# Performance work log

Hardware: AMD Instinct MI355X
Metric: run time of the kernel (lower is better)

## Reference

```python
import jax, jax.numpy as jnp
import numpy as np

B, T, E, H, V = 32, 120, 300, 256, 32000
C, G = 512, 7

def setup_inputs() -> dict:
    key = jax.random.key(0)
    ks = jax.random.split(key, 8)
    s = lambda k, shape, sc: (jax.random.normal(k, shape, jnp.float32) * sc)
    return {
        "features": jax.random.normal(ks[0], (B, C, G, G), jnp.float32),
        "embeddings": jax.random.normal(ks[1], (B, T, E), jnp.float32),
        "W_init": s(ks[2], (H, C), 0.04),          # nn.Linear(512, num_layers*H)
        "b_init": jnp.zeros((H,), jnp.float32),
        "W_fc2": s(ks[3], (H, C * G * G), 0.006),   # nn.Linear(512*49, H)
        "b_fc2": jnp.zeros((H,), jnp.float32),
        "W_ih": s(ks[4], (3 * H, E + H), 0.04),     # GRU weight_ih_l0 (r,z,n rows)
        "b_ih": jnp.zeros((3 * H,), jnp.float32),
        "W_hh": s(ks[5], (3 * H, H), 0.06),         # GRU weight_hh_l0
        "b_hh": jnp.zeros((3 * H,), jnp.float32),
        "W_fc": s(ks[6], (V, H), 0.06),             # nn.Linear(H, vocab)
        "b_fc": jnp.zeros((V,), jnp.float32),
        "length": T,
    }

def reference(features, embeddings, W_init, b_init, W_fc2, b_fc2,
              W_ih, b_ih, W_hh, b_hh, W_fc, b_fc, length):
    Bq, Cq = features.shape[0], features.shape[1]
    Hq = W_hh.shape[1]
    # init_hidden_state: [B,C,7,7] -> [B,49,C]
    f = jnp.transpose(features, (0, 2, 3, 1)).reshape(Bq, -1, Cq)
    h0 = f.mean(axis=1) @ W_init.T + b_init                      # [B,H], num_layers=1
    # flatten + fc2, broadcast over time, concat with embeddings
    feat = f.reshape(Bq, -1) @ W_fc2.T + b_fc2                   # [B,H]
    x = jnp.concatenate(
        [embeddings,
         jnp.broadcast_to(feat[:, None, :], (Bq, embeddings.shape[1], Hq))],
        axis=-1)                                                  # [B,T,E+H]
    xs = jnp.transpose(x[:, :length], (1, 0, 2))                  # [T,B,E+H]
    # precompute input-side gate projections for all timesteps (one big GEMM)
    gi = jnp.einsum('tbi,gi->tbg', xs, W_ih) + b_ih               # [T,B,3H]
    def step(h, g_x):
        g_h = h @ W_hh.T + b_hh
        r = jax.nn.sigmoid(g_x[..., :Hq] + g_h[..., :Hq])
        z = jax.nn.sigmoid(g_x[..., Hq:2 * Hq] + g_h[..., Hq:2 * Hq])
        n = jnp.tanh(g_x[..., 2 * Hq:] + r * g_h[..., 2 * Hq:])
        h_new = (1.0 - z) * n + z * h
        return h_new, h_new
    _, hs = jax.lax.scan(step, h0, gi)                            # [T,B,H]
    # per-step fc (dropout p=0.3 is identity in eval mode)
    logits = jnp.einsum('tbh,vh->btv', hs, W_fc) + b_fc           # [B,T,V]
    return logits
```

## Files before the change

### kernel.cpp

```cpp
#include <hip/hip_runtime.h>
#include <hip/hip_bf16.h>

#define BB 32
#define TT 120
#define EE 300
#define HH 256
#define VV 32000
#define CC 512
#define GG 49
#define KIN 556
#define CF 25088

typedef __attribute__((ext_vector_type(8))) short bf16x8;
typedef __attribute__((ext_vector_type(4))) float f32x4;

__device__ __forceinline__ float bpair_lo(unsigned int u) { return __uint_as_float(u << 16); }
__device__ __forceinline__ float bpair_hi(unsigned int u) { return __uint_as_float(u & 0xFFFF0000u); }

__device__ __forceinline__ unsigned int packbf(float a, float b) {
    union { __hip_bfloat16 h; unsigned short u; } ua, ub;
    ua.h = __float2bfloat16(a); ub.h = __float2bfloat16(b);
    return (unsigned int)ua.u | ((unsigned int)ub.u << 16);
}

#if defined(__has_builtin)
#  if __has_builtin(__builtin_amdgcn_fdot2_f32_bf16)
#    define USE_DOT2 1
#  endif
#endif
#ifndef USE_DOT2
#  define USE_DOT2 0
#endif

#if USE_DOT2
typedef __bf16 bf2_t __attribute__((ext_vector_type(2)));
__device__ __forceinline__ float dot2bf(unsigned int w, unsigned int h, float c) {
    return __builtin_amdgcn_fdot2_f32_bf16(__builtin_bit_cast(bf2_t, w),
                                           __builtin_bit_cast(bf2_t, h), c, false);
}
#else
__device__ __forceinline__ float dot2bf(unsigned int w, unsigned int h, float c) {
    c = fmaf(bpair_lo(w), bpair_lo(h), c);
    c = fmaf(bpair_hi(w), bpair_hi(h), c);
    return c;
}
#endif

__global__ void __launch_bounds__(256) k_pre(const float* __restrict__ features,
                                             const float* __restrict__ W_fc2,
                                             float* __restrict__ part,
                                             const float* __restrict__ W_hh,
                                             unsigned int* __restrict__ whh_bf,
                                             const float* __restrict__ W_init,
                                             const float* __restrict__ b_init,
                                             float* __restrict__ h0) {
    __shared__ float xs[98][BB];
    __shared__ float mf[CC];
    __shared__ float red[8][33];
    int bid = blockIdx.x;
    if (bid < 256) {
        int kc = bid;
        for (int idx = threadIdx.x; idx < 98 * BB; idx += 256) {
            int ii = idx >> 5, b = idx & 31;
            int ig = kc * 98 + ii;
            int c = ig & 511, p = ig >> 9;
            xs[ii][b] = features[(size_t)b * CF + c * GG + p];
        }
        __syncthreads();
        int h = threadIdx.x;
        float acc[BB];
#pragma unroll
        for (int b = 0; b < BB; ++b) acc[b] = 0.f;
        const float* wp = W_fc2 + (size_t)h * CF + kc * 98;
        for (int ii = 0; ii < 98; ii += 2) {
            float2 w2 = *(const float2*)(wp + ii);
            const float4* x0 = (const float4*)&xs[ii][0];
            const float4* x1 = (const float4*)&xs[ii + 1][0];
#pragma unroll
            for (int q = 0; q < 8; ++q) {
                float4 a4 = x0[q], b4 = x1[q];
                acc[4 * q + 0] += w2.x * a4.x + w2.y * b4.x;
                acc[4 * q + 1] += w2.x * a4.y + w2.y * b4.y;
                acc[4 * q + 2] += w2.x * a4.z + w2.y * b4.z;
                acc[4 * q + 3] += w2.x * a4.w + w2.y * b4.w;
            }
        }
        float* pp = part + (size_t)kc * (BB * 256) + h;
#pragma unroll
        for (int b = 0; b < BB; ++b) pp[b * 256] = acc[b];
    } else if (bid < 640) {
        int idx = (bid - 256) * 256 + threadIdx.x;
        float2 w2 = *(const float2*)(W_hh + (size_t)idx * 2);
        whh_bf[idx] = packbf(w2.x, w2.y);
    } else {
        int lb = bid - 640;
        int b  = lb >> 3;
        int hc = lb & 7;
        {
            const float* p = features + (size_t)b * CF + (size_t)threadIdx.x * 2 * GG;
            float s0 = 0.f, s1 = 0.f;
#pragma unroll
            for (int i = 0; i < GG; ++i) s0 += p[i];
#pragma unroll
            for (int i = 0; i < GG; ++i) s1 += p[GG + i];
            mf[threadIdx.x * 2]     = s0 * (1.0f / 49.0f);
            mf[threadIdx.x * 2 + 1] = s1 * (1.0f / 49.0f);
        }
        __syncthreads();
        int h  = threadIdx.x & 31;
        int kg = threadIdx.x >> 5;
        int gh = hc * 32 + h;
        const float* w = W_init + (size_t)gh * CC + kg * 64;
        const float* m = mf + kg * 64;
        float s = 0.f;
#pragma unroll
        for (int k = 0; k < 64; k += 4) {
            float4 w4 = *(const float4*)(w + k);
            s += m[k] * w4.x + m[k + 1] * w4.y + m[k + 2] * w4.z + m[k + 3] * w4.w;
        }
        red[kg][h] = s;
        __syncthreads();
        if (threadIdx.x < 32) {
            float t = b_init[hc * 32 + threadIdx.x];
#pragma unroll
            for (int g = 0; g < 8; ++g) t += red[g][threadIdx.x];
            h0[b * HH + hc * 32 + threadIdx.x] = t;
        }
    }
}

__global__ void __launch_bounds__(256) k_fc2b(const float* __restrict__ part,
                                              const float* __restrict__ b_fc2,
                                              float* __restrict__ feat) {
    int b  = blockIdx.x;
    int hc = blockIdx.y;
    int h  = threadIdx.x & 31;
    int kg = threadIdx.x >> 5;
    int gh = hc * 32 + h;
    __shared__ float red[8][33];
    const float* pp = part + (size_t)kg * 32 * (BB * 256) + b * 256 + gh;
    float s = 0.f;
#pragma unroll
    for (int kc = 0; kc < 32; ++kc) s += pp[(size_t)kc * (BB * 256)];
    red[kg][h] = s;
    __syncthreads();
    if (threadIdx.x < 32) {
        float t = b_fc2[hc * 32 + threadIdx.x];
#pragma unroll
        for (int g = 0; g < 8; ++g) t += red[g][threadIdx.x];
        feat[b * HH + hc * 32 + threadIdx.x] = t;
    }
}

__global__ void __launch_bounds__(256) k_gi(const float* __restrict__ emb,
                                            const float* __restrict__ feat,
                                            const float* __restrict__ W_ih,
                                            const float* __restrict__ b_ih,
                                            float* __restrict__ gi) {
    __shared__ float As[64][68];
    __shared__ float Bs[64][68];
    int n0 = blockIdx.x * 64;
    int m0 = blockIdx.y * 64;
    int tid = threadIdx.x;
    int tm = (tid & 15) * 4;
    int tn = (tid >> 4) * 4;
    float acc[4][4] = {};

    int mrA[4], klA[4];
#pragma unroll
    for (int s = 0; s < 4; ++s) {
        int slot = tid * 4 + s;
        mrA[s] = slot >> 4;
        klA[s] = (slot & 15) * 4;
    }

    float4 ra[4], rb[4];

#define LOADG(KC)                                                                 \
    do {                                                                          \
        int k0_ = (KC) * 64;                                                      \
        _Pragma("unroll") for (int s = 0; s < 4; ++s) {                           \
            int m = m0 + mrA[s];                                                  \
            int t = m >> 5, b = m & 31;                                           \
            int kg = k0_ + klA[s];                                                \
            if (kg + 4 <= EE) {                                                   \
                ra[s] = *(const float4*)(emb + ((size_t)b * TT + t) * EE + kg);   \
            } else if (kg >= EE && kg + 4 <= KIN) {                               \
                ra[s] = *(const float4*)(feat + (size_t)b * HH + (kg - EE));      \
            } else {                                                              \
                float tmp[4];                                                     \
                _Pragma("unroll") for (int q = 0; q < 4; ++q) {                   \
                    int kq = kg + q;                                              \
                    tmp[q] = (kq < EE) ? emb[((size_t)b * TT + t) * EE + kq]      \
                           : (kq < KIN) ? feat[(size_t)b * HH + (kq - EE)] : 0.f; \
                }                                                                 \
                ra[s] = *(float4*)tmp;                                            \
            }                                                                     \
        }                                                                         \
        _Pragma("unroll") for (int s = 0; s < 4; ++s) {                           \
            int gidx = n0 + mrA[s];                                               \
            int kg = k0_ + klA[s];                                                \
            if (kg + 4 <= KIN) {                                                  \
                rb[s] = *(const float4*)(W_ih + (size_t)gidx * KIN + kg);         \
            } else {                                                              \
                float tmp[4];                                                     \
                _Pragma("unroll") for (int q = 0; q < 4; ++q) {                   \
                    int kq = kg + q;                                              \
                    tmp[q] = (kq < KIN) ? W_ih[(size_t)gidx * KIN + kq] : 0.f;    \
                }                                                                 \
                rb[s] = *(float4*)tmp;                                            \
            }                                                                     \
        }                                                                         \
    } while (0)

#define STORES()                                                                  \
    do {                                                                          \
        _Pragma("unroll") for (int s = 0; s < 4; ++s) {                           \
            As[klA[s] + 0][mrA[s]] = ra[s].x;                                     \
            As[klA[s] + 1][mrA[s]] = ra[s].y;                                     \
            As[klA[s] + 2][mrA[s]] = ra[s].z;                                     \
            As[klA[s] + 3][mrA[s]] = ra[s].w;                                     \
            Bs[klA[s] + 0][mrA[s]] = rb[s].x;                                     \
            Bs[klA[s] + 1][mrA[s]] = rb[s].y;                                     \
            Bs[klA[s] + 2][mrA[s]] = rb[s].z;                                     \
            Bs[klA[s] + 3][mrA[s]] = rb[s].w;                                     \
        }                                                                         \
    } while (0)

    LOADG(0);
#pragma unroll 1
    for (int kc = 0; kc < 9; ++kc) {
        __syncthreads();
        STORES();
        if (kc < 8) LOADG(kc + 1);
        __syncthreads();
        int kmax = (kc == 8) ? 44 : 64;
        for (int k = 0; k < kmax; ++k) {
            float4 av = *(const float4*)&As[k][tm];
            float4 bv = *(const float4*)&Bs[k][tn];
            const float* ap = (const float*)&av;
            const float* bp = (const float*)&bv;
#pragma unroll
            for (int i = 0; i < 4; ++i)
#pragma unroll
                for (int j = 0; j < 4; ++j)
                    acc[i][j] = fmaf(ap[i], bp[j], acc[i][j]);
        }
    }
#undef LOADG
#undef STORES

    float4 bias = *(const float4*)(b_ih + n0 + tn);
    const float* bp = (const float*)&bias;
#pragma unroll
    for (int i = 0; i < 4; ++i) {
        int m = m0 + tm + i;
        float4 o;
        o.x = acc[i][0] + bp[0];
        o.y = acc[i][1] + bp[1];
        o.z = acc[i][2] + bp[2];
        o.w = acc[i][3] + bp[3];
        *(float4*)(gi + (size_t)m * 768 + n0 + tn) = o;
    }
}

__device__ __forceinline__ void gru_body(int b, const float* __restrict__ h0,
                                         const float* __restrict__ gi,
                                         const unsigned int* __restrict__ whh_bf,
                                         const float* __restrict__ b_hh,
                                         __hip_bfloat16* __restrict__ hA,
                                         unsigned int* h_pk, float* hf,
                                         float* r_sh, float* z_sh) {
    int jp = threadIdx.x;
    int j  = jp & 255;
    int g  = jp >> 8;
    const unsigned int* wr = whh_bf + (size_t)jp * 128;
    float bias = b_hh[jp];
    if (jp < HH) hf[jp] = h0[b * HH + jp];
    __syncthreads();
    if (jp < 128) h_pk[jp] = packbf(hf[2 * jp], hf[2 * jp + 1]);
    __syncthreads();

    for (int t = 0; t < TT; ++t) {
        float a0 = 0.f, a1 = 0.f, a2 = 0.f, a3 = 0.f;
#pragma unroll
        for (int kk = 0; kk < 128; kk += 4) {
            uint4 wq = *(const uint4*)(wr + kk);
            uint4 hq = *(const uint4*)&h_pk[kk];
            a0 = dot2bf(wq.x, hq.x, a0);
            a1 = dot2bf(wq.y, hq.y, a1);
            a2 = dot2bf(wq.z, hq.z, a2);
            a3 = dot2bf(wq.w, hq.w, a3);
        }
        float a = (a0 + a1) + (a2 + a3);
        float gx = gi[((size_t)t * BB + b) * 768 + jp];
        if (g == 0)      r_sh[j] = 1.f / (1.f + __expf(-(gx + a + bias)));
        else if (g == 1) z_sh[j] = 1.f / (1.f + __expf(-(gx + a + bias)));
        __syncthreads();
        if (g == 2) {
            float n  = tanhf(gx + r_sh[j] * (a + bias));
            float z  = z_sh[j];
            float hn = (1.f - z) * n + z * hf[j];
            hf[j] = hn;
            hA[((size_t)b * TT + t) * HH + j] = __float2bfloat16(hn);
        }
        __syncthreads();
        if (jp < 128) h_pk[jp] = packbf(hf[2 * jp], hf[2 * jp + 1]);
        __syncthreads();
    }
}

__global__ void __launch_bounds__(768, 3) k_gru(const float* __restrict__ h0,
                                                const float* __restrict__ gi,
                                                const unsigned int* __restrict__ whh_bf,
                                                const float* __restrict__ b_hh,
                                                __hip_bfloat16* __restrict__ hA) {
    __shared__ unsigned int h_pk[128];
    __shared__ float hf[256];
    __shared__ float r_sh[256];
    __shared__ float z_sh[256];
    gru_body(blockIdx.x, h0, gi, whh_bf, b_hh, hA, h_pk, hf, r_sh, z_sh);
}

#define CVT_N4 2048000
__global__ void __launch_bounds__(768, 3) k_gru_cvt(const float* __restrict__ h0,
                                                    const float* __restrict__ gi,
                                                    const unsigned int* __restrict__ whh_bf,
                                                    const float* __restrict__ b_hh,
                                                    __hip_bfloat16* __restrict__ hA,
                                                    const float* __restrict__ W_fc,
                                                    __hip_bfloat16* __restrict__ wfc) {
    if (blockIdx.x >= 32) {
        size_t base = (size_t)(blockIdx.x - 32) * (768 * 4) + threadIdx.x;
#pragma unroll
        for (int q = 0; q < 4; ++q) {
            size_t fi = base + (size_t)q * 768;
            if (fi < CVT_N4) {
                float4 v = *((const float4*)W_fc + fi);
                __hip_bfloat16 o[4];
                o[0] = __float2bfloat16(v.x);
                o[1] = __float2bfloat16(v.y);
                o[2] = __float2bfloat16(v.z);
                o[3] = __float2bfloat16(v.w);
                *((uint2*)wfc + fi) = *(uint2*)o;
            }
        }
        return;
    }
    __shared__ unsigned int h_pk[128];
    __shared__ float hf[256];
    __shared__ float r_sh[256];
    __shared__ float z_sh[256];
    gru_body(blockIdx.x, h0, gi, whh_bf, b_hh, hA, h_pk, hf, r_sh, z_sh);
}

__global__ void k_cvt(const float* __restrict__ src, __hip_bfloat16* __restrict__ dst) {
    size_t i = ((size_t)blockIdx.x * 256 + threadIdx.x) * 4;
    float4 v = *(const float4*)(src + i);
    __hip_bfloat16 o[4];
    o[0] = __float2bfloat16(v.x);
    o[1] = __float2bfloat16(v.y);
    o[2] = __float2bfloat16(v.z);
    o[3] = __float2bfloat16(v.w);
    *(uint2*)(dst + i) = *(uint2*)o;
}

__global__ void __launch_bounds__(512) k_logits(const __hip_bfloat16* __restrict__ hA,
                                                const __hip_bfloat16* __restrict__ wfc,
                                                const float* __restrict__ b_fc,
                                                float* __restrict__ out) {
    __shared__ short As[256][64];
    __shared__ short Bs[128][64];
    char* AsB = (char*)As;
    char* BsB = (char*)Bs;

    int nt = blockIdx.x;
    int mt = blockIdx.y;
    int tid  = threadIdx.x;
    int wave = tid >> 6, lane = tid & 63;
    int wm = wave >> 1;
    int wn = wave & 1;
    int lr = lane & 15;
    int lk = lane >> 4;

    int rs = tid >> 3;
    int cs = tid & 7;
    const short* Ag = (const short*)hA  + ((size_t)mt * 256 + rs) * HH + cs * 8;
    const short* Bg = (const short*)wfc + ((size_t)nt * 128 + rs) * HH + cs * 8;
    int wofsA[4], wofsB[2];
#pragma unroll
    for (int s = 0; s < 4; ++s) {
        int row = s * 64 + rs;
        wofsA[s] = row * 128 + ((cs ^ (row & 7)) * 16);
    }
#pragma unroll
    for (int s = 0; s < 2; ++s) {
        int row = s * 64 + rs;
        wofsB[s] = row * 128 + ((cs ^ (row & 7)) * 16);
    }

    f32x4 acc[4][4] = {};

#define LOADT(kt, GA, GB)                                                        \
    do {                                                                         \
        _Pragma("unroll") for (int s = 0; s < 4; ++s)                            \
            GA[s] = *(const bf16x8*)(Ag + (size_t)s * 64 * HH + (kt) * 64);      \
        _Pragma("unroll") for (int s = 0; s < 2; ++s)                            \
            GB[s] = *(const bf16x8*)(Bg + (size_t)s * 64 * HH + (kt) * 64);      \
    } while (0)

#define STORET(GA, GB)                                                           \
    do {                                                                         \
        _Pragma("unroll") for (int s = 0; s < 4; ++s)                            \
            *(bf16x8*)(AsB + wofsA[s]) = GA[s];                                  \
        _Pragma("unroll") for (int s = 0; s < 2; ++s)                            \
            *(bf16x8*)(BsB + wofsB[s]) = GB[s];                                  \
    } while (0)

#define COMPUTE()                                                                \
    do {                                                                         \
        _Pragma("unroll") for (int kk = 0; kk < 2; ++kk) {                       \
            bf16x8 af[4], bg[4];                                                 \
            _Pragma("unroll") for (int i = 0; i < 4; ++i) {                      \
                int r = wm * 64 + i * 16 + lr;                                   \
                af[i] = *(const bf16x8*)(AsB + r * 128 + (((kk * 4 + lk) ^ (r & 7)) * 16)); \
            }                                                                    \
            _Pragma("unroll") for (int j = 0; j < 4; ++j) {                      \
                int r = wn * 64 + j * 16 + lr;                                   \
                bg[j] = *(const bf16x8*)(BsB + r * 128 + (((kk * 4 + lk) ^ (r & 7)) * 16)); \
            }                                                                    \
            _Pragma("unroll") for (int i = 0; i < 4; ++i)                        \
                _Pragma("unroll") for (int j = 0; j < 4; ++j)                    \
                    acc[i][j] = __builtin_amdgcn_mfma_f32_16x16x32_bf16(af[i], bg[j], acc[i][j], 0, 0, 0); \
        }                                                                        \
    } while (0)

    bf16x8 gA[4], gB[2], gA2[4], gB2[2];
    LOADT(0, gA, gB);
    STORET(gA, gB);   LOADT(1, gA2, gB2); __syncthreads(); COMPUTE(); __syncthreads();
    STORET(gA2, gB2); LOADT(2, gA, gB);   __syncthreads(); COMPUTE(); __syncthreads();
    STORET(gA, gB);   LOADT(3, gA2, gB2); __syncthreads(); COMPUTE(); __syncthreads();
    STORET(gA2, gB2);                     __syncthreads(); COMPUTE();

#undef LOADT
#undef STORET
#undef COMPUTE

    int m_base = mt * 256 + wm * 64;
    int n_base = nt * 128 + wn * 64;
#pragma unroll
    for (int i = 0; i < 4; ++i) {
#pragma unroll
        for (int j = 0; j < 4; ++j) {
            int v = n_base + j * 16 + lr;
            float bias = b_fc[v];
#pragma unroll
            for (int q = 0; q < 4; ++q) {
                int m = m_base + i * 16 + lk * 4 + q;
                out[(size_t)m * VV + v] = acc[i][j][q] + bias;
            }
        }
    }
}

extern "C" void kernel_launch(void* const* d_in, const int* in_sizes, int n_in,
                              void* d_out, int out_size, void* d_ws, size_t ws_size,
                              hipStream_t stream) {
    (void)in_sizes; (void)n_in; (void)out_size;
    const float* features   = (const float*)d_in[0];
    const float* embeddings = (const float*)d_in[1];
    const float* W_init     = (const float*)d_in[2];
    const float* b_init     = (const float*)d_in[3];
    const float* W_fc2      = (const float*)d_in[4];
    const float* b_fc2      = (const float*)d_in[5];
    const float* W_ih       = (const float*)d_in[6];
    const float* b_ih       = (const float*)d_in[7];
    const float* W_hh       = (const float*)d_in[8];
    const float* b_hh       = (const float*)d_in[9];
    const float* W_fc       = (const float*)d_in[10];
    const float* b_fc       = (const float*)d_in[11];

    char* ws = (char*)d_ws;
    float* feat   = (float*)(ws + 65536);
    float* hbuf0  = (float*)(ws + 98304);
    __hip_bfloat16* hA = (__hip_bfloat16*)(ws + 131072);
    float* gi     = (float*)(ws + 2097152);
    float* part   = (float*)(ws + 2097152);
    unsigned int* whh_bf = (unsigned int*)(ws + 13893632);
    float* outp = (float*)d_out;

    int fused = (ws_size >= 30670848u);
    __hip_bfloat16* wfc = fused ? (__hip_bfloat16*)(ws + 14286848)
                                : (__hip_bfloat16*)(ws + 2097152);

    k_pre<<<896, 256, 0, stream>>>(features, W_fc2, part, W_hh, whh_bf, W_init, b_init, hbuf0);
    k_fc2b<<<dim3(32, 8), 256, 0, stream>>>(part, b_fc2, feat);
    k_gi<<<dim3(12, 60), 256, 0, stream>>>(embeddings, feat, W_ih, b_ih, gi);
    if (fused) {
        k_gru_cvt<<<32 + 667, 768, 0, stream>>>(hbuf0, gi, whh_bf, b_hh, hA, W_fc, wfc);
    } else {
        k_gru<<<32, 768, 0, stream>>>(hbuf0, gi, whh_bf, b_hh, hA);
        k_cvt<<<8000, 256, 0, stream>>>(W_fc, wfc);
    }
    k_logits<<<dim3(250, 15), 512, 0, stream>>>(hA, wfc, b_fc, outp);
}
```

Baseline: 400.0 us.

## Split input-gate GEMM, computing embedding part inside the prologue kernel

The input-gate projection is split along K. The embedding half (K=300) is now computed by extra blocks of k_pre, so it runs alongside the fc2 partial sums and W_hh conversion. A new k_gi2 kernel computes only the feature half (K=256) after feat is ready, then adds its result and the bias onto the stored gi values. The fc2 partial buffer moves into the unused tail of the output buffer, since gi is now live during k_pre; the logits kernel overwrites that region later. The goal is to take part of the serial GEMM off the critical path. In exchange, gi gets an extra read-modify-write pass, and the embedding path loses its register double-buffering.

New measurement: 394.2 us. About the same (-1.4%).

```diff
diff --git a/kernel.cpp b/kernel.cpp
--- a/kernel.cpp
+++ b/kernel.cpp
@@ -53,21 +53,24 @@
                                              unsigned int* __restrict__ whh_bf,
                                              const float* __restrict__ W_init,
                                              const float* __restrict__ b_init,
-                                             float* __restrict__ h0) {
-    __shared__ float xs[98][BB];
-    __shared__ float mf[CC];
-    __shared__ float red[8][33];
+                                             float* __restrict__ h0,
+                                             const float* __restrict__ emb,
+                                             const float* __restrict__ W_ih,
+                                             float* __restrict__ gi) {
+    __shared__ __align__(16) char smem[2 * 64 * 68 * 4];
     int bid = blockIdx.x;
+    int tid = threadIdx.x;
     if (bid < 256) {
+        float (*xs)[BB] = (float(*)[BB])smem;
         int kc = bid;
-        for (int idx = threadIdx.x; idx < 98 * BB; idx += 256) {
+        for (int idx = tid; idx < 98 * BB; idx += 256) {
             int ii = idx >> 5, b = idx & 31;
             int ig = kc * 98 + ii;
             int c = ig & 511, p = ig >> 9;
             xs[ii][b] = features[(size_t)b * CF + c * GG + p];
         }
         __syncthreads();
-        int h = threadIdx.x;
+        int h = tid;
         float acc[BB];
 #pragma unroll
         for (int b = 0; b < BB; ++b) acc[b] = 0.f;
@@ -88,27 +91,111 @@
         float* pp = part + (size_t)kc * (BB * 256) + h;
 #pragma unroll
         for (int b = 0; b < BB; ++b) pp[b * 256] = acc[b];
-    } else if (bid < 640) {
-        int idx = (bid - 256) * 256 + threadIdx.x;
+    } else if (bid < 976) {
+        float (*As)[68] = (float(*)[68])smem;
+        float (*Bs)[68] = (float(*)[68])(smem + 17408);
+        int idx = bid - 256;
+        int n0 = (idx % 12) * 64;
+        int m0 = (idx / 12) * 64;
+        int tm = (tid & 15) * 4;
+        int tn = (tid >> 4) * 4;
+        float acc[4][4] = {};
+        int mrA[4], klA[4];
+#pragma unroll
+        for (int s = 0; s < 4; ++s) {
+            int slot = tid * 4 + s;
+            mrA[s] = slot >> 4;
+            klA[s] = (slot & 15) * 4;
+        }
+        float4 ra[4], rb[4];
+#pragma unroll 1
+        for (int kc = 0; kc < 5; ++kc) {
+            int k0 = kc * 64;
+#pragma unroll
+            for (int s = 0; s < 4; ++s) {
+                int m = m0 + mrA[s];
+                int t = m >> 5, b = m & 31;
+                int kg = k0 + klA[s];
+                if (kg + 4 <= EE) {
+                    ra[s] = *(const float4*)(emb + ((size_t)b * TT + t) * EE + kg);
+                } else {
+                    float tmp[4];
+#pragma unroll
+                    for (int q = 0; q < 4; ++q) {
+                        int kq = kg + q;
+                        tmp[q] = (kq < EE) ? emb[((size_t)b * TT + t) * EE + kq] : 0.f;
+                    }
+                    ra[s] = *(float4*)tmp;
+                }
+                int gidx = n0 + mrA[s];
+                if (kg + 4 <= EE) {
+                    rb[s] = *(const float4*)(W_ih + (size_t)gidx * KIN + kg);
+                } else {
+                    float tmp[4];
+#pragma unroll
+                    for (int q = 0; q < 4; ++q) {
+                        int kq = kg + q;
+                        tmp[q] = (kq < EE) ? W_ih[(size_t)gidx * KIN + kq] : 0.f;
+                    }
+                    rb[s] = *(float4*)tmp;
+                }
+            }
+            __syncthreads();
+#pragma unroll
+            for (int s = 0; s < 4; ++s) {
+                As[klA[s] + 0][mrA[s]] = ra[s].x;
+                As[klA[s] + 1][mrA[s]] = ra[s].y;
+                As[klA[s] + 2][mrA[s]] = ra[s].z;
+                As[klA[s] + 3][mrA[s]] = ra[s].w;
+                Bs[klA[s] + 0][mrA[s]] = rb[s].x;
+                Bs[klA[s] + 1][mrA[s]] = rb[s].y;
+                Bs[klA[s] + 2][mrA[s]] = rb[s].z;
+                Bs[klA[s] + 3][mrA[s]] = rb[s].w;
+            }
+            __syncthreads();
+            int kmax = (kc == 4) ? 44 : 64;
+            for (int k = 0; k < kmax; ++k) {
+                float4 av = *(const float4*)&As[k][tm];
+                float4 bv = *(const float4*)&Bs[k][tn];
+                const float* ap = (const float*)&av;
+                const float* bp = (const float*)&bv;
+#pragma unroll
+                for (int i = 0; i < 4; ++i)
+#pragma unroll
+                    for (int j = 0; j < 4; ++j)
+                        acc[i][j] = fmaf(ap[i], bp[j], acc[i][j]);
+            }
+        }
+#pragma unroll
+        for (int i = 0; i < 4; ++i) {
+            int m = m0 + tm + i;
+            float4 o;
+            o.x = acc[i][0]; o.y = acc[i][1]; o.z = acc[i][2]; o.w = acc[i][3];
+            *(float4*)(gi + (size_t)m * 768 + n0 + tn) = o;
+        }
+    } else if (bid < 1360) {
+        int idx = (bid - 976) * 256 + tid;
         float2 w2 = *(const float2*)(W_hh + (size_t)idx * 2);
         whh_bf[idx] = packbf(w2.x, w2.y);
     } else {
-        int lb = bid - 640;
+        float* mf = (float*)smem;
+        float (*red)[33] = (float(*)[33])(smem + 2048);
+        int lb = bid - 1360;
         int b  = lb >> 3;
         int hc = lb & 7;
         {
-            const float* p = features + (size_t)b * CF + (size_t)threadIdx.x * 2 * GG;
+            const float* p = features + (size_t)b * CF + (size_t)tid * 2 * GG;
             float s0 = 0.f, s1 = 0.f;
 #pragma unroll
             for (int i = 0; i < GG; ++i) s0 += p[i];
 #pragma unroll
             for (int i = 0; i < GG; ++i) s1 += p[GG + i];
-            mf[threadIdx.x * 2]     = s0 * (1.0f / 49.0f);
-            mf[threadIdx.x * 2 + 1] = s1 * (1.0f / 49.0f);
-        }
-        __syncthreads();
-        int h  = threadIdx.x & 31;
-        int kg = threadIdx.x >> 5;
+            mf[tid * 2]     = s0 * (1.0f / 49.0f);
+            mf[tid * 2 + 1] = s1 * (1.0f / 49.0f);
+        }
+        __syncthreads();
+        int h  = tid & 31;
+        int kg = tid >> 5;
         int gh = hc * 32 + h;
         const float* w = W_init + (size_t)gh * CC + kg * 64;
         const float* m = mf + kg * 64;
@@ -120,11 +207,11 @@
         }
         red[kg][h] = s;
         __syncthreads();
-        if (threadIdx.x < 32) {
-            float t = b_init[hc * 32 + threadIdx.x];
-#pragma unroll
-            for (int g = 0; g < 8; ++g) t += red[g][threadIdx.x];
-            h0[b * HH + hc * 32 + threadIdx.x] = t;
+        if (tid < 32) {
+            float t = b_init[hc * 32 + tid];
+#pragma unroll
+            for (int g = 0; g < 8; ++g) t += red[g][tid];
+            h0[b * HH + hc * 32 + tid] = t;
         }
     }
 }
@@ -152,11 +239,10 @@
     }
 }
 
-__global__ void __launch_bounds__(256) k_gi(const float* __restrict__ emb,
-                                            const float* __restrict__ feat,
-                                            const float* __restrict__ W_ih,
-                                            const float* __restrict__ b_ih,
-                                            float* __restrict__ gi) {
+__global__ void __launch_bounds__(256) k_gi2(const float* __restrict__ feat,
+                                             const float* __restrict__ W_ih,
+                                             const float* __restrict__ b_ih,
+                                             float* __restrict__ gi) {
     __shared__ float As[64][68];
     __shared__ float Bs[64][68];
     int n0 = blockIdx.x * 64;
@@ -165,7 +251,6 @@
     int tm = (tid & 15) * 4;
     int tn = (tid >> 4) * 4;
     float acc[4][4] = {};
-
     int mrA[4], klA[4];
 #pragma unroll
     for (int s = 0; s < 4; ++s) {
@@ -173,69 +258,32 @@
         mrA[s] = slot >> 4;
         klA[s] = (slot & 15) * 4;
     }
-
     float4 ra[4], rb[4];
-
-#define LOADG(KC)                                                                 \
-    do {                                                                          \
-        int k0_ = (KC) * 64;                                                      \
-        _Pragma("unroll") for (int s = 0; s < 4; ++s) {                           \
-            int m = m0 + mrA[s];                                                  \
-            int t = m >> 5, b = m & 31;                                           \
-            int kg = k0_ + klA[s];                                                \
-            if (kg + 4 <= EE) {                                                   \
-                ra[s] = *(const float4*)(emb + ((size_t)b * TT + t) * EE + kg);   \
-            } else if (kg >= EE && kg + 4 <= KIN) {                               \
-                ra[s] = *(const float4*)(feat + (size_t)b * HH + (kg - EE));      \
-            } else {                                                              \
-                float tmp[4];                                                     \
-                _Pragma("unroll") for (int q = 0; q < 4; ++q) {                   \
-                    int kq = kg + q;                                              \
-                    tmp[q] = (kq < EE) ? emb[((size_t)b * TT + t) * EE + kq]      \
-                           : (kq < KIN) ? feat[(size_t)b * HH + (kq - EE)] : 0.f; \
-                }                                                                 \
-                ra[s] = *(float4*)tmp;                                            \
-            }                                                                     \
-        }                                                                         \
-        _Pragma("unroll") for (int s = 0; s < 4; ++s) {                           \
-            int gidx = n0 + mrA[s];                                               \
-            int kg = k0_ + klA[s];                                                \
-            if (kg + 4 <= KIN) {                                                  \
-                rb[s] = *(const float4*)(W_ih + (size_t)gidx * KIN + kg);         \
-            } else {                                                              \
-                float tmp[4];                                                     \
-                _Pragma("unroll") for (int q = 0; q < 4; ++q) {                   \
-                    int kq = kg + q;                                              \
-                    tmp[q] = (kq < KIN) ? W_ih[(size_t)gidx * KIN + kq] : 0.f;    \
-                }                                                                 \
-                rb[s] = *(float4*)tmp;                                            \
-            }                                                                     \
-        }                                                                         \
-    } while (0)
-
-#define STORES()                                                                  \
-    do {                                                                          \
-        _Pragma("unroll") for (int s = 0; s < 4; ++s) {                           \
-            As[klA[s] + 0][mrA[s]] = ra[s].x;                                     \
-            As[klA[s] + 1][mrA[s]] = ra[s].y;                                     \
-            As[klA[s] + 2][mrA[s]] = ra[s].z;                                     \
-            As[klA[s] + 3][mrA[s]] = ra[s].w;                                     \
-            Bs[klA[s] + 0][mrA[s]] = rb[s].x;                                     \
-            Bs[klA[s] + 1][mrA[s]] = rb[s].y;                                     \
-            Bs[klA[s] + 2][mrA[s]] = rb[s].z;                                     \
-            Bs[klA[s] + 3][mrA[s]] = rb[s].w;                                     \
-        }                                                                         \
-    } while (0)
-
-    LOADG(0);
 #pragma unroll 1
-    for (int kc = 0; kc < 9; ++kc) {
-        __syncthreads();
-        STORES();
-        if (kc < 8) LOADG(kc + 1);
-        __syncthreads();
-        int kmax = (kc == 8) ? 44 : 64;
-        for (int k = 0; k < kmax; ++k) {
+    for (int kc = 0; kc < 4; ++kc) {
+        int k0 = EE + kc * 64;
+#pragma unroll
+        for (int s = 0; s < 4; ++s) {
+            int m = m0 + mrA[s];
+            int b = m & 31;
+            int kg = k0 + klA[s];
+            ra[s] = *(const float4*)(feat + (size_t)b * HH + (kg - EE));
+            rb[s] = *(const float4*)(W_ih + (size_t)(n0 + mrA[s]) * KIN + kg);
+        }
+        __syncthreads();
+#pragma unroll
+        for (int s = 0; s < 4; ++s) {
+            As[klA[s] + 0][mrA[s]] = ra[s].x;
+            As[klA[s] + 1][mrA[s]] = ra[s].y;
+            As[klA[s] + 2][mrA[s]] = ra[s].z;
+            As[klA[s] + 3][mrA[s]] = ra[s].w;
+            Bs[klA[s] + 0][mrA[s]] = rb[s].x;
+            Bs[klA[s] + 1][mrA[s]] = rb[s].y;
+            Bs[klA[s] + 2][mrA[s]] = rb[s].z;
+            Bs[klA[s] + 3][mrA[s]] = rb[s].w;
+        }
+        __syncthreads();
+        for (int k = 0; k < 64; ++k) {
             float4 av = *(const float4*)&As[k][tm];
             float4 bv = *(const float4*)&Bs[k][tn];
             const float* ap = (const float*)&av;
@@ -247,19 +295,17 @@
                     acc[i][j] = fmaf(ap[i], bp[j], acc[i][j]);
         }
     }
-#undef LOADG
-#undef STORES
-
     float4 bias = *(const float4*)(b_ih + n0 + tn);
     const float* bp = (const float*)&bias;
 #pragma unroll
     for (int i = 0; i < 4; ++i) {
         int m = m0 + tm + i;
+        float4 prev = *(const float4*)(gi + (size_t)m * 768 + n0 + tn);
         float4 o;
-        o.x = acc[i][0] + bp[0];
-        o.y = acc[i][1] + bp[1];
-        o.z = acc[i][2] + bp[2];
-        o.w = acc[i][3] + bp[3];
+        o.x = prev.x + acc[i][0] + bp[0];
+        o.y = prev.y + acc[i][1] + bp[1];
+        o.z = prev.z + acc[i][2] + bp[2];
+        o.w = prev.w + acc[i][3] + bp[3];
         *(float4*)(gi + (size_t)m * 768 + n0 + tn) = o;
     }
 }
@@ -485,17 +531,18 @@
     float* hbuf0  = (float*)(ws + 98304);
     __hip_bfloat16* hA = (__hip_bfloat16*)(ws + 131072);
     float* gi     = (float*)(ws + 2097152);
-    float* part   = (float*)(ws + 2097152);
     unsigned int* whh_bf = (unsigned int*)(ws + 13893632);
     float* outp = (float*)d_out;
+    float* part = (float*)d_out + 120782848;
 
     int fused = (ws_size >= 30670848u);
     __hip_bfloat16* wfc = fused ? (__hip_bfloat16*)(ws + 14286848)
                                 : (__hip_bfloat16*)(ws + 2097152);
 
-    k_pre<<<896, 256, 0, stream>>>(features, W_fc2, part, W_hh, whh_bf, W_init, b_init, hbuf0);
+    k_pre<<<1616, 256, 0, stream>>>(features, W_fc2, part, W_hh, whh_bf, W_init, b_init,
+                                    hbuf0, embeddings, W_ih, gi);
     k_fc2b<<<dim3(32, 8), 256, 0, stream>>>(part, b_fc2, feat);
-    k_gi<<<dim3(12, 60), 256, 0, stream>>>(embeddings, feat, W_ih, b_ih, gi);
+    k_gi2<<<dim3(12, 60), 256, 0, stream>>>(feat, W_ih, b_ih, gi);
     if (fused) {
         k_gru_cvt<<<32 + 667, 768, 0, stream>>>(hbuf0, gi, whh_bf, b_hh, hA, W_fc, wfc);
     } else {
```
